# Kernel optimization log

Hardware: AMD Instinct MI355X
Metric: run time of the kernel (lower is better)

## Reference

```python
import jax, jax.numpy as jnp
import numpy as np

UP = 2

def _rect_1d(N, cutoff, edge_val):
    # ideal LPF rect in frequency domain (as in alias_free_convnets ideal_lpf.py)
    lo = int((N * cutoff) // 2)
    hi = int(N - lo)
    r = np.ones(N, dtype=np.float32)
    r[lo + 1:hi] = 0.0
    if (cutoff * N) % 2 == 0:
        r[lo] = edge_val
        r[hi] = edge_val
    return r

def _rect_mask_rfft(N, cutoff, edge_val):
    # 2D separable rect mask, cropped to rfft width N//2+1 (assumes square HxW)
    r = _rect_1d(N, cutoff, edge_val)
    m = r[:, None] * r[None, :]
    return jnp.asarray(m[:, :N // 2 + 1])

def _upsample_rfft(x):
    # x: [B, C, H, W] channels-first. Zero-insertion upsample by UP, then
    # ideal reconstruction LPF in rfft domain (recon rect has edge value 1).
    B, C, H, W = x.shape
    z = jnp.zeros((B, C, H, UP, W, UP), x.dtype)
    z = z.at[:, :, :, 0, :, 0].set(x)
    xu = z.reshape(B, C, H * UP, W * UP)
    mask = _rect_mask_rfft(W * UP, 1.0 / UP, 1.0)
    xf = jnp.fft.rfft2(xu) * (UP * UP) * mask
    return jnp.fft.irfft2(xf, s=(H * UP, W * UP)).astype(x.dtype)

def _lpf_rfft(x, cutoff=0.5):
    # ideal low-pass filter in rfft domain (lpf rect has edge value 0.5)
    H, W = x.shape[-2], x.shape[-1]
    mask = _rect_mask_rfft(W, cutoff, 0.5)
    xf = jnp.fft.rfft2(x) * mask
    return jnp.fft.irfft2(xf, s=(H, W)).astype(x.dtype)

def setup_inputs() -> dict:
    key = jax.random.key(0)
    ks = jax.random.split(key, 6)
    B, H, W, dim = 16, 64, 64, 96
    hidden = 4 * dim  # expand_ratio * dim
    x = jax.random.normal(ks[0], (B, H, W, dim), jnp.float32)
    W1 = jax.random.normal(ks[1], (hidden, dim), jnp.float32) * 0.02
    b1 = jnp.zeros((hidden,), jnp.float32)
    W2 = jax.random.normal(ks[2], (dim, hidden), jnp.float32) * 0.02
    b2 = jnp.zeros((dim,), jnp.float32)
    # PolyActPerChannel default coefficients, repeated per channel: [hidden, 3]
    init_coef = jnp.asarray([0.0169394634313126, 0.5, 0.3078363963999393], jnp.float32)
    coef = jnp.tile(init_coef[None, :], (hidden, 1))
    return {"x": x, "W1": W1, "b1": b1, "W2": W2, "b2": b2, "coef": coef}

def reference(x, W1, b1, W2, b2, coef):
    # x: [B, H, W, C] channels-last
    xc = jnp.transpose(x, (0, 3, 1, 2))            # [B, C, H, W]
    xu = _upsample_rfft(xc)                        # [B, C, 2H, 2W]
    h = jnp.transpose(xu, (0, 2, 3, 1))            # [B, 2H, 2W, C]
    h = h @ W1.T + b1                              # pwconv1 -> [B, 2H, 2W, 4C]
    # per-channel degree-2 polynomial activation
    h = coef[:, 0] + coef[:, 1] * h + coef[:, 2] * (h * h)
    h = h @ W2.T + b2                              # pwconv2 -> [B, 2H, 2W, C]
    hc = jnp.transpose(h, (0, 3, 1, 2))            # [B, C, 2H, 2W]
    hl = _lpf_rfft(hc, cutoff=0.5)                 # anti-alias LPF
    out = hl[:, :, ::2, ::2]                       # stride-2 downsample
    return jnp.transpose(out, (0, 2, 3, 1))        # [B, H, W, C]
```

## Files before the change

kernel.cpp:

```cpp
#include <hip/hip_runtime.h>
#include <hip/hip_bf16.h>

typedef __hip_bfloat16 bf16;
typedef __bf16 bf16x8 __attribute__((ext_vector_type(8)));
typedef float f32x16 __attribute__((ext_vector_type(16)));

union Frag { uint4 q; bf16x8 v; unsigned short us[8]; };

#define PI_D 3.14159265358979323846

__device__ __forceinline__ unsigned short bfbits(float x){ bf16 h = __float2bfloat16(x); return *(unsigned short*)&h; }
__device__ __forceinline__ float frombits(unsigned short b){ union{float f; unsigned u;}v; v.u = ((unsigned)b)<<16; return v.f; }

#define GLD_LDS16(gp, lp) __builtin_amdgcn_global_load_lds( \
    (const __attribute__((address_space(1))) unsigned int*)(gp), \
    (__attribute__((address_space(3))) unsigned int*)(lp), 16, 0, 0)

__global__ void k_init(const float* __restrict__ W1, const float* __restrict__ b1,
                       const float* __restrict__ W2, const float* __restrict__ b2,
                       const float* __restrict__ coef,
                       bf16* __restrict__ W1f, bf16* __restrict__ W2A2f,
                       float* __restrict__ rtab, float* __restrict__ bias2p) {
    int idx = blockIdx.x * 256 + threadIdx.x;
    if (idx < 96) {
        float acc = b2[idx];
        for (int h = 0; h < 384; ++h) {
            float bb = b1[h], C0 = coef[h*3], C1 = coef[h*3+1], C2 = coef[h*3+2];
            float A0 = C0 + C1 * bb + C2 * bb * bb;
            acc += W2[idx * 384 + h] * A0;
        }
        bias2p[idx] = acc;
    }
    if (idx < 384) {
        float bb = b1[idx], C1 = coef[idx*3+1], C2 = coef[idx*3+2];
        rtab[idx] = (C1 + 2.f * C2 * bb) / C2;
    }
    if (idx < 36864) {
        int j = idx & 7, lane = (idx >> 3) & 63, rest = idx >> 9;
        int g2 = lane >> 5;
        {
            int s = rest % 6, ht = rest / 6;
            int p = lane & 31;
            int b = p >> 2, m4 = b & 3; if (m4 == 1 || m4 == 2) b ^= 3;
            int h = ht * 32 + ((b << 2) | (p & 3));
            int k = s * 16 + g2 * 8 + j;
            W1f[idx] = __float2bfloat16(W1[h * 96 + k]);
        }
        {
            int s = rest & 1, rest2 = rest >> 1;
            int ct = rest2 % 3, ht = rest2 / 3;
            int c = ct * 32 + (lane & 31);
            int h = ht * 32 + s * 16 + g2 * 8 + j;
            float C2 = coef[h*3+2];
            W2A2f[idx] = __float2bfloat16(W2[c * 384 + h] * C2);
        }
    }
}

__global__ void k_init2(bf16* __restrict__ upA, bf16* __restrict__ lpA) {
    int idx = blockIdx.x * 256 + threadIdx.x;
    int e = (idx < 12288) ? idx : idx - 12288;
    int j = e & 7, lane = (e >> 3) & 63, mt = (e >> 9) & 1, step = e >> 10;
    int m = 32 * mt + (lane & 31);
    int p = (step & 3) * 16 + (lane >> 5) * 8 + j;
    int d2 = 2 * (m - p);
    int n = ((idx < 12288) ? (d2 + 1) : (d2 - 1)) & 127;
    double s = 1.0;
    for (int k = 1; k <= 31; ++k) s += 2.0 * cos((2.0 * PI_D / 128.0) * (double)k * (double)n);
    float F = (float)(s / ((idx < 12288) ? 64.0 : 128.0));
    bf16 fh = __float2bfloat16(F);
    bf16 val = (step < 8) ? fh : __float2bfloat16(F - __bfloat162float(fh));
    (idx < 12288 ? upA : lpA)[((step * 2 + mt) * 64 + lane) * 8 + j] = val;
}

__device__ __forceinline__ void fir_load_a12(const uint4* __restrict__ atab,
                                             int lane, int mt, Frag af[12]) {
    #pragma unroll
    for (int s = 0; s < 12; ++s) af[s].q = atab[(s * 2 + mt) * 64 + lane];
}
__device__ __forceinline__ void fir_load_a8(const uint4* __restrict__ atab,
                                            int lane, int mt, Frag af[8]) {
    #pragma unroll
    for (int s = 0; s < 8; ++s) {
        int st = (s < 4) ? s : (s + 4);
        af[s].q = atab[(st * 2 + mt) * 64 + lane];
    }
}

__device__ __forceinline__ f32x16 fir_gemm(const Frag af[12],
                                           const unsigned char* BtS,
                                           int lane, int nt) {
    const int n = 32 * nt + (lane & 31);
    const int rowbase = n * 256;
    const int swz = (n & 7) << 4;
    const int g16 = (lane >> 5) * 16;
    f32x16 C;
    #pragma unroll
    for (int e = 0; e < 16; ++e) C[e] = 0.f;
    #pragma unroll
    for (int s = 0; s < 12; ++s) {
        int k2 = (s & 3) * 32 + (((s >> 2) == 1) ? 128 : 0) + g16;
        Frag bf_;
        bf_.q = *(const uint4*)(BtS + rowbase + (k2 ^ swz));
        C = __builtin_amdgcn_mfma_f32_32x32x16_bf16(af[s].v, bf_.v, C, 0, 0, 0);
    }
    return C;
}

__device__ __forceinline__ f32x16 fir_gemm_h(const Frag af[8],
                                             const unsigned char* BtS,
                                             int lane, int nt) {
    const int n = 32 * nt + (lane & 31);
    const int rowbase = n * 128;
    const int swz = (n & 7) << 4;
    const int g16 = (lane >> 5) * 16;
    f32x16 C;
    #pragma unroll
    for (int e = 0; e < 16; ++e) C[e] = 0.f;
    #pragma unroll
    for (int s = 0; s < 8; ++s) {
        int k2 = (s & 3) * 32 + g16;
        Frag bf_;
        bf_.q = *(const uint4*)(BtS + rowbase + (k2 ^ swz));
        C = __builtin_amdgcn_mfma_f32_32x32x16_bf16(af[s].v, bf_.v, C, 0, 0, 0);
    }
    return C;
}

__global__ __launch_bounds__(384, 2) void k_up_v(const float* __restrict__ x,
                                                 const uint4* __restrict__ atab,
                                                 bf16* __restrict__ t1) {
    __shared__ __align__(16) unsigned char BtS[24576];
    __shared__ __align__(16) float xe[64 * 96];
    __shared__ float As[96];
    const int tid = threadIdx.x;
    const int lane = tid & 63, w = tid >> 6;
    const int b = blockIdx.x >> 6, q = blockIdx.x & 63;
    Frag af[12];
    fir_load_a12(atab, lane, w / 3, af);
    for (int g = tid; g < 768; g += 384) {
        int pp = g / 24, c4 = (g - pp * 24) * 4;
        const float* xsrc = &x[((b * 64 + 2 * pp) * 64 + q) * 96 + c4];
        float4 v0 = *(const float4*)xsrc;
        float4 v1 = *(const float4*)(xsrc + 6144);
        *(float4*)&xe[(2 * pp) * 96 + c4] = v0;
        *(float4*)&xe[(2 * pp + 1) * 96 + c4] = v1;
        float f0a[4] = {v0.x, v0.y, v0.z, v0.w};
        float f1a[4] = {v1.x, v1.y, v1.z, v1.w};
        #pragma unroll
        for (int e = 0; e < 4; ++e) {
            int n = c4 + e;
            unsigned short h0 = bfbits(f0a[e]), h1 = bfbits(f1a[e]);
            unsigned short l0 = bfbits(f0a[e] - frombits(h0));
            unsigned short l1 = bfbits(f1a[e] - frombits(h1));
            int base = n * 256 + ((4 * pp) ^ ((n & 7) << 4));
            *(unsigned*)(BtS + base) = (unsigned)h0 | ((unsigned)h1 << 16);
            *(unsigned*)(BtS + base + 128) = (unsigned)l0 | ((unsigned)l1 << 16);
        }
    }
    __syncthreads();
    if (tid < 96) {
        float a = 0.f;
        for (int p = 0; p < 64; p += 2) a += xe[p * 96 + tid] - xe[(p + 1) * 96 + tid];
        As[tid] = a * 0.015625f;
    }
    __syncthreads();
    f32x16 C = fir_gemm(af, BtS, lane, w % 3);
    bf16* dst = t1 + (size_t)b * 786432 + (size_t)q * 96;
    const int c = 32 * (w % 3) + (lane & 31);
    #pragma unroll
    for (int r = 0; r < 16; ++r) {
        int m = 32 * (w / 3) + (r & 3) + 8 * (r >> 2) + 4 * (lane >> 5);
        dst[(size_t)(2 * m + 1) * 6144 + c] = __float2bfloat16(C[r]);
    }
    for (int g = tid; g < 1536; g += 384) {
        int u = g / 24, c4 = (g - u * 24) * 4;
        float sgn = (u & 1) ? -1.f : 1.f;
        float4 xv = *(const float4*)&xe[u * 96 + c4];
        float4 av = *(const float4*)&As[c4];
        uint2 pk;
        pk.x = (unsigned)bfbits(fmaf(sgn, av.x, xv.x)) | ((unsigned)bfbits(fmaf(sgn, av.y, xv.y)) << 16);
        pk.y = (unsigned)bfbits(fmaf(sgn, av.z, xv.z)) | ((unsigned)bfbits(fmaf(sgn, av.w, xv.w)) << 16);
        *(uint2*)&dst[(size_t)(2 * u) * 6144 + c4] = pk;
    }
}

__global__ __launch_bounds__(384, 2) void k_up_h(const bf16* __restrict__ t1,
                                                 const uint4* __restrict__ atab,
                                                 bf16* __restrict__ xu) {
    __shared__ __align__(16) unsigned char BtS[96 * 128];
    __shared__ __align__(16) bf16 xe[64 * 96];
    __shared__ float As[96];
    const int tid = threadIdx.x;
    const int lane = tid & 63, w = tid >> 6;
    const size_t row = blockIdx.x;
    const bf16* src = t1 + row * 6144;
    Frag af[8];
    fir_load_a8(atab, lane, w / 3, af);
    {
        int pp = tid / 12, c8 = (tid - pp * 12) * 8;
        const bf16* s0 = src + (2 * pp) * 96 + c8;
        uint4 v0 = *(const uint4*)s0;
        uint4 v1 = *(const uint4*)(s0 + 96);
        *(uint4*)&xe[(2 * pp) * 96 + c8] = v0;
        *(uint4*)&xe[(2 * pp + 1) * 96 + c8] = v1;
        const unsigned short* u0 = (const unsigned short*)&v0;
        const unsigned short* u1 = (const unsigned short*)&v1;
        #pragma unroll
        for (int e = 0; e < 8; ++e) {
            int n = c8 + e;
            int base = n * 128 + ((4 * pp) ^ ((n & 7) << 4));
            *(unsigned*)(BtS + base) = (unsigned)u0[e] | ((unsigned)u1[e] << 16);
        }
    }
    __syncthreads();
    if (tid < 96) {
        float a = 0.f;
        for (int p = 0; p < 64; p += 2)
            a += __bfloat162float(xe[p * 96 + tid]) - __bfloat162float(xe[(p + 1) * 96 + tid]);
        As[tid] = a * 0.015625f;
    }
    __syncthreads();
    f32x16 C = fir_gemm_h(af, BtS, lane, w % 3);
    bf16* dst = xu + row * 12288;
    const int c = 32 * (w % 3) + (lane & 31);
    #pragma unroll
    for (int r = 0; r < 16; ++r) {
        int m = 32 * (w / 3) + (r & 3) + 8 * (r >> 2) + 4 * (lane >> 5);
        dst[(2 * m + 1) * 96 + c] = __float2bfloat16(C[r]);
    }
    for (int g = tid; g < 1536; g += 384) {
        int v = g / 24, c4 = (g - v * 24) * 4;
        float sgn = (v & 1) ? -1.f : 1.f;
        uint2 xv = *(const uint2*)&xe[v * 96 + c4];
        const unsigned short* us = (const unsigned short*)&xv;
        uint2 pk;
        pk.x = (unsigned)bfbits(fmaf(sgn, As[c4 + 0], frombits(us[0])))
             | ((unsigned)bfbits(fmaf(sgn, As[c4 + 1], frombits(us[1]))) << 16);
        pk.y = (unsigned)bfbits(fmaf(sgn, As[c4 + 2], frombits(us[2])))
             | ((unsigned)bfbits(fmaf(sgn, As[c4 + 3], frombits(us[3]))) << 16);
        *(uint2*)&dst[(2 * v) * 96 + c4] = pk;
    }
}

__global__ __launch_bounds__(512, 2) void k_mlp(const bf16* __restrict__ xu,
                                                const uint4* __restrict__ W1f,
                                                const uint4* __restrict__ W2A2f,
                                                const float* __restrict__ rtabg,
                                                const float* __restrict__ bias2p,
                                                bf16* __restrict__ y) {
    extern __shared__ __align__(16) uint4 wAll[];
    float* rtabL = (float*)(wAll + 144 * 64);
    const int tid = threadIdx.x;
    const int lane = tid & 63;
    const int w = tid >> 6;
    const int half = w & 1;
    const int rw = w >> 1;
    const int lm = lane & 31;
    const int g = lane >> 5;
    const size_t row = (size_t)blockIdx.x * 4 + rw;

    #pragma unroll 2
    for (int c0 = 0; c0 < 144; c0 += 8) {
        int c = c0 + w;
        const uint4* gp = (c < 72) ? (W1f + (size_t)c * 64)
                                   : (W2A2f + (size_t)(c - 72) * 64);
        GLD_LDS16(gp + lane, &wAll[c * 64]);
    }
    if (tid < 96) GLD_LDS16(rtabg + tid * 4, rtabL + tid * 4);

    Frag xr0[6], xr1[6];
    const bf16* xb0 = xu + row * 12288 + (size_t)(half * 64 + lm) * 96 + g * 8;
    const bf16* xb1 = xb0 + 32 * 96;
    #pragma unroll
    for (int s = 0; s < 6; ++s) { xr0[s].q = *(const uint4*)(xb0 + 16 * s);
                                  xr1[s].q = *(const uint4*)(xb1 + 16 * s); }

    asm volatile("s_waitcnt vmcnt(0)" ::: "memory");
    __syncthreads();

    f32x16 ya0[3], ya1[3];
    #pragma unroll
    for (int ct = 0; ct < 3; ++ct) {
        #pragma unroll
        for (int e = 0; e < 16; ++e) { ya0[ct][e] = 0.f; ya1[ct][e] = 0.f; }
    }

    for (int ht = 0; ht < 12; ++ht) {
        const float* rt = rtabL + ht * 32 + g * 8;
        float4 r00 = *(const float4*)(rt);
        float4 r01 = *(const float4*)(rt + 4);
        float4 r10 = *(const float4*)(rt + 16);
        float4 r11 = *(const float4*)(rt + 20);
        float rr[16] = {r00.x, r00.y, r00.z, r00.w, r01.x, r01.y, r01.z, r01.w,
                        r10.x, r10.y, r10.z, r10.w, r11.x, r11.y, r11.z, r11.w};
        f32x16 d0, d1;
        #pragma unroll
        for (int e = 0; e < 16; ++e) { d0[e] = 0.f; d1[e] = 0.f; }
        #pragma unroll
        for (int s = 0; s < 6; ++s) {
            Frag a; a.q = wAll[(ht * 6 + s) * 64 + lane];
            d0 = __builtin_amdgcn_mfma_f32_32x32x16_bf16(a.v, xr0[s].v, d0, 0, 0, 0);
            d1 = __builtin_amdgcn_mfma_f32_32x32x16_bf16(a.v, xr1[s].v, d1, 0, 0, 0);
        }
        Frag be0[2], be1[2];
        #pragma unroll
        for (int s2 = 0; s2 < 2; ++s2) {
            #pragma unroll
            for (int j = 0; j < 8; ++j) {
                float rv = rr[s2 * 8 + j];
                float v0 = d0[s2 * 8 + j], v1 = d1[s2 * 8 + j];
                be0[s2].v[j] = (__bf16)(v0 * (v0 + rv));
                be1[s2].v[j] = (__bf16)(v1 * (v1 + rv));
            }
        }
        #pragma unroll
        for (int u = 0; u < 6; ++u) {
            int ct = u >> 1, s2 = u & 1;
            Frag a2; a2.q = wAll[(72 + ht * 6 + u) * 64 + lane];
            ya0[ct] = __builtin_amdgcn_mfma_f32_32x32x16_bf16(a2.v, (s2 ? be0[1] : be0[0]).v, ya0[ct], 0, 0, 0);
            ya1[ct] = __builtin_amdgcn_mfma_f32_32x32x16_bf16(a2.v, (s2 ? be1[1] : be1[0]).v, ya1[ct], 0, 0, 0);
        }
    }
    bf16* yb0 = y + row * 12288 + (size_t)(half * 64 + lm) * 96;
    bf16* yb1 = yb0 + 32 * 96;
    #pragma unroll
    for (int ct = 0; ct < 3; ++ct) {
        #pragma unroll
        for (int t = 0; t < 8; ++t) {
            int cbase = 32 * ct + 8 * (t >> 1) + 2 * (t & 1) + 4 * g;
            float bb0 = bias2p[cbase], bb1 = bias2p[cbase + 1];
            unsigned pk0 = (unsigned)bfbits(ya0[ct][2*t] + bb0) | ((unsigned)bfbits(ya0[ct][2*t+1] + bb1) << 16);
            unsigned pk1 = (unsigned)bfbits(ya1[ct][2*t] + bb0) | ((unsigned)bfbits(ya1[ct][2*t+1] + bb1) << 16);
            *(unsigned*)(yb0 + cbase) = pk0;
            *(unsigned*)(yb1 + cbase) = pk1;
        }
    }
}

__global__ __launch_bounds__(384, 2) void k_lpf_v(const bf16* __restrict__ y,
                                                  const uint4* __restrict__ atab,
                                                  bf16* __restrict__ t2) {
    __shared__ __align__(16) unsigned char BtS[192 * 128];
    __shared__ __align__(16) bf16 xe[64 * 192];
    const int tid = threadIdx.x;
    const int lane = tid & 63, w = tid >> 6;
    const int b = blockIdx.x >> 6, j2 = blockIdx.x & 63;
    for (int g = tid; g < 1536; g += 384) {
        int ie = g / 24, rem = g - ie * 24, col = rem / 12, c8 = (rem - col * 12) * 8;
        uint4 v = *(const uint4*)(y + ((size_t)((b * 128 + 2 * ie) * 128 + 2 * j2 + col)) * 96 + c8);
        *(uint4*)&xe[ie * 192 + col * 96 + c8] = v;
    }
    for (int g = tid; g < 768; g += 384) {
        int q_ = g / 24, rem = g - q_ * 24, col = rem / 12, c8 = (rem - col * 12) * 8;
        const bf16* yb = y + ((size_t)((b * 128 + 4 * q_ + 1) * 128 + 2 * j2 + col)) * 96 + c8;
        uint4 v0 = *(const uint4*)yb;
        uint4 v1 = *(const uint4*)(yb + 2 * 12288);
        int np = col * 96 + c8;
        const unsigned short* u0 = (const unsigned short*)&v0;
        const unsigned short* u1 = (const unsigned short*)&v1;
        #pragma unroll
        for (int e = 0; e < 8; ++e) {
            int n = np + e;
            int base = n * 128 + ((4 * q_) ^ ((n & 7) << 4));
            *(unsigned*)(BtS + base) = (unsigned)u0[e] | ((unsigned)u1[e] << 16);
        }
    }
    __syncthreads();
    const int n = 32 * w + (lane & 31);
    const int rowbase = n * 128;
    const int swz = (n & 7) << 4;
    const int g16 = (lane >> 5) * 16;
    f32x16 C0, C1;
    #pragma unroll
    for (int e = 0; e < 16; ++e) { C0[e] = 0.f; C1[e] = 0.f; }
    #pragma unroll
    for (int s = 0; s < 4; ++s) {
        Frag bf_; bf_.q = *(const uint4*)(BtS + rowbase + ((s * 32 + g16) ^ swz));
        Frag a0h; a0h.q = atab[(s * 2 + 0) * 64 + lane];
        Frag a1h; a1h.q = atab[(s * 2 + 1) * 64 + lane];
        Frag a0l; a0l.q = atab[((8 + s) * 2 + 0) * 64 + lane];
        Frag a1l; a1l.q = atab[((8 + s) * 2 + 1) * 64 + lane];
        C0 = __builtin_amdgcn_mfma_f32_32x32x16_bf16(a0h.v, bf_.v, C0, 0, 0, 0);
        C1 = __builtin_amdgcn_mfma_f32_32x32x16_bf16(a1h.v, bf_.v, C1, 0, 0, 0);
        C0 = __builtin_amdgcn_mfma_f32_32x32x16_bf16(a0l.v, bf_.v, C0, 0, 0, 0);
        C1 = __builtin_amdgcn_mfma_f32_32x32x16_bf16(a1l.v, bf_.v, C1, 0, 0, 0);
    }
    const int col = n / 96;
    const int c = n - col * 96;
    const int j = 2 * j2 + col;
    #pragma unroll
    for (int r = 0; r < 16; ++r) {
        int mrow = (r & 3) + 8 * (r >> 2) + 4 * (lane >> 5);
        t2[(size_t)((b * 64 + mrow) * 128 + j) * 96 + c] =
            __float2bfloat16(C0[r] + 0.5f * __bfloat162float(xe[mrow * 192 + n]));
        t2[(size_t)((b * 64 + 32 + mrow) * 128 + j) * 96 + c] =
            __float2bfloat16(C1[r] + 0.5f * __bfloat162float(xe[(32 + mrow) * 192 + n]));
    }
}

__global__ __launch_bounds__(384, 2) void k_lpf_h(const bf16* __restrict__ t2,
                                                  const uint4* __restrict__ atab,
                                                  float* __restrict__ out) {
    __shared__ __align__(16) unsigned char BtS[96 * 128];
    __shared__ __align__(16) bf16 xe[64 * 96];
    const int tid = threadIdx.x;
    const int lane = tid & 63, w = tid >> 6;
    const size_t row = blockIdx.x;
    const bf16* src = t2 + row * 12288;
    Frag af[8];
    fir_load_a8(atab, lane, w / 3, af);
    for (int g = tid; g < 768; g += 384) {
        int ce = g / 12, c8 = (g - ce * 12) * 8;
        uint4 v = *(const uint4*)(src + (2 * ce) * 96 + c8);
        *(uint4*)&xe[ce * 96 + c8] = v;
    }
    {
        int q_ = tid / 12, c8 = (tid - q_ * 12) * 8;
        const bf16* s0 = src + (4 * q_ + 1) * 96 + c8;
        uint4 v0 = *(const uint4*)s0;
        uint4 v1 = *(const uint4*)(s0 + 2 * 96);
        const unsigned short* u0 = (const unsigned short*)&v0;
        const unsigned short* u1 = (const unsigned short*)&v1;
        #pragma unroll
        for (int e = 0; e < 8; ++e) {
            int n = c8 + e;
            int base = n * 128 + ((4 * q_) ^ ((n & 7) << 4));
            *(unsigned*)(BtS + base) = (unsigned)u0[e] | ((unsigned)u1[e] << 16);
        }
    }
    __syncthreads();
    f32x16 C = fir_gemm_h(af, BtS, lane, w % 3);
    const int c = 32 * (w % 3) + (lane & 31);
    #pragma unroll
    for (int r = 0; r < 16; ++r) {
        int m = 32 * (w / 3) + (r & 3) + 8 * (r >> 2) + 4 * (lane >> 5);
        out[row * 6144 + (size_t)m * 96 + c] = C[r] + 0.5f * __bfloat162float(xe[m * 96 + c]);
    }
}

extern "C" void kernel_launch(void* const* d_in, const int* in_sizes, int n_in,
                              void* d_out, int out_size, void* d_ws, size_t ws_size,
                              hipStream_t stream) {
    const float* x    = (const float*)d_in[0];
    const float* W1   = (const float*)d_in[1];
    const float* b1   = (const float*)d_in[2];
    const float* W2   = (const float*)d_in[3];
    const float* b2   = (const float*)d_in[4];
    const float* coef = (const float*)d_in[5];
    float* out = (float*)d_out;

    char* w = (char*)d_ws;
    float* bias2p = (float*)(w);
    bf16*  W1f    = (bf16*)(w + 512);
    bf16*  W2A2f  = (bf16*)(w + 74240);
    float* rtab   = (float*)(w + 147968);
    bf16*  atabU  = (bf16*)(w + 149504);
    bf16*  atabL  = (bf16*)(w + 174080);
    bf16* t1 = (bf16*)(w + 270848);
    bf16* yv = (bf16*)(w + 270848);
    bf16* xu = (bf16*)(w + 100934144);
    bf16* t2 = (bf16*)(w + 100934144);

    k_init <<<144, 256, 0, stream>>>(W1, b1, W2, b2, coef, W1f, W2A2f, rtab, bias2p);
    k_init2<<<96, 256, 0, stream>>>(atabU, atabL);
    k_up_v <<<1024, 384, 0, stream>>>(x, (const uint4*)atabU, t1);
    k_up_h <<<2048, 384, 0, stream>>>(t1, (const uint4*)atabU, xu);
    k_mlp  <<<512, 512, 148992, stream>>>(xu, (const uint4*)W1f, (const uint4*)W2A2f,
                                          rtab, bias2p, yv);
    k_lpf_v<<<1024, 384, 0, stream>>>(yv, (const uint4*)atabL, t2);
    k_lpf_h<<<1024, 384, 0, stream>>>(t2, (const uint4*)atabL, out);
}
```

Before: 143.0 us.

## Halve MLP kernel LDS and per-wave tile, read W2 fragments from global

The MLP kernel now stages only W1 fragments and the activation table in shared memory, roughly halving LDS use. W2 fragments are read per iteration from global memory, relying on L2/L1 caching. Each wave now handles one 32-row tile instead of two, each block covers 2 rows instead of 4, and the grid doubles. The goal is higher occupancy (launch bounds raised to 4 blocks) and lower register pressure. The cost is repeated global loads of W2 per wave and less reuse of each weight fragment across MFMAs.

```diff
diff --git a/kernel.cpp b/kernel.cpp
--- a/kernel.cpp
+++ b/kernel.cpp
@@ -243,97 +243,79 @@
     }
 }
 
-__global__ __launch_bounds__(512, 2) void k_mlp(const bf16* __restrict__ xu,
+__global__ __launch_bounds__(512, 4) void k_mlp(const bf16* __restrict__ xu,
                                                 const uint4* __restrict__ W1f,
                                                 const uint4* __restrict__ W2A2f,
                                                 const float* __restrict__ rtabg,
                                                 const float* __restrict__ bias2p,
                                                 bf16* __restrict__ y) {
     extern __shared__ __align__(16) uint4 wAll[];
-    float* rtabL = (float*)(wAll + 144 * 64);
+    float* rtabL = (float*)(wAll + 72 * 64);
     const int tid = threadIdx.x;
     const int lane = tid & 63;
     const int w = tid >> 6;
-    const int half = w & 1;
-    const int rw = w >> 1;
+    const int rw = w >> 2;
+    const int mt = w & 3;
     const int lm = lane & 31;
     const int g = lane >> 5;
-    const size_t row = (size_t)blockIdx.x * 4 + rw;
-
-    #pragma unroll 2
-    for (int c0 = 0; c0 < 144; c0 += 8) {
-        int c = c0 + w;
-        const uint4* gp = (c < 72) ? (W1f + (size_t)c * 64)
-                                   : (W2A2f + (size_t)(c - 72) * 64);
-        GLD_LDS16(gp + lane, &wAll[c * 64]);
-    }
+    const size_t row = (size_t)blockIdx.x * 2 + rw;
+
+    for (int c = w; c < 72; c += 8)
+        GLD_LDS16(W1f + c * 64 + lane, &wAll[c * 64]);
     if (tid < 96) GLD_LDS16(rtabg + tid * 4, rtabL + tid * 4);
 
-    Frag xr0[6], xr1[6];
-    const bf16* xb0 = xu + row * 12288 + (size_t)(half * 64 + lm) * 96 + g * 8;
-    const bf16* xb1 = xb0 + 32 * 96;
-    #pragma unroll
-    for (int s = 0; s < 6; ++s) { xr0[s].q = *(const uint4*)(xb0 + 16 * s);
-                                  xr1[s].q = *(const uint4*)(xb1 + 16 * s); }
+    Frag xr[6];
+    const bf16* xb = xu + row * 12288 + (size_t)(mt * 32 + lm) * 96 + g * 8;
+    #pragma unroll
+    for (int s = 0; s < 6; ++s) xr[s].q = *(const uint4*)(xb + 16 * s);
 
     asm volatile("s_waitcnt vmcnt(0)" ::: "memory");
     __syncthreads();
 
-    f32x16 ya0[3], ya1[3];
+    f32x16 ya[3];
     #pragma unroll
     for (int ct = 0; ct < 3; ++ct) {
         #pragma unroll
-        for (int e = 0; e < 16; ++e) { ya0[ct][e] = 0.f; ya1[ct][e] = 0.f; }
+        for (int e = 0; e < 16; ++e) ya[ct][e] = 0.f;
     }
 
     for (int ht = 0; ht < 12; ++ht) {
-        const float* rt = rtabL + ht * 32 + g * 8;
-        float4 r00 = *(const float4*)(rt);
-        float4 r01 = *(const float4*)(rt + 4);
-        float4 r10 = *(const float4*)(rt + 16);
-        float4 r11 = *(const float4*)(rt + 20);
-        float rr[16] = {r00.x, r00.y, r00.z, r00.w, r01.x, r01.y, r01.z, r01.w,
-                        r10.x, r10.y, r10.z, r10.w, r11.x, r11.y, r11.z, r11.w};
-        f32x16 d0, d1;
-        #pragma unroll
-        for (int e = 0; e < 16; ++e) { d0[e] = 0.f; d1[e] = 0.f; }
+        Frag a2f[6];
+        #pragma unroll
+        for (int u = 0; u < 6; ++u) a2f[u].q = W2A2f[(ht * 6 + u) * 64 + lane];
+        f32x16 d;
+        #pragma unroll
+        for (int e = 0; e < 16; ++e) d[e] = 0.f;
         #pragma unroll
         for (int s = 0; s < 6; ++s) {
             Frag a; a.q = wAll[(ht * 6 + s) * 64 + lane];
-            d0 = __builtin_amdgcn_mfma_f32_32x32x16_bf16(a.v, xr0[s].v, d0, 0, 0, 0);
-            d1 = __builtin_amdgcn_mfma_f32_32x32x16_bf16(a.v, xr1[s].v, d1, 0, 0, 0);
-        }
-        Frag be0[2], be1[2];
+            d = __builtin_amdgcn_mfma_f32_32x32x16_bf16(a.v, xr[s].v, d, 0, 0, 0);
+        }
+        Frag be[2];
         #pragma unroll
         for (int s2 = 0; s2 < 2; ++s2) {
             #pragma unroll
             for (int j = 0; j < 8; ++j) {
-                float rv = rr[s2 * 8 + j];
-                float v0 = d0[s2 * 8 + j], v1 = d1[s2 * 8 + j];
-                be0[s2].v[j] = (__bf16)(v0 * (v0 + rv));
-                be1[s2].v[j] = (__bf16)(v1 * (v1 + rv));
+                float rv = rtabL[ht * 32 + s2 * 16 + g * 8 + j];
+                float v0 = d[s2 * 8 + j];
+                be[s2].v[j] = (__bf16)(v0 * (v0 + rv));
             }
         }
         #pragma unroll
         for (int u = 0; u < 6; ++u) {
-            int ct = u >> 1, s2 = u & 1;
-            Frag a2; a2.q = wAll[(72 + ht * 6 + u) * 64 + lane];
-            ya0[ct] = __builtin_amdgcn_mfma_f32_32x32x16_bf16(a2.v, (s2 ? be0[1] : be0[0]).v, ya0[ct], 0, 0, 0);
-            ya1[ct] = __builtin_amdgcn_mfma_f32_32x32x16_bf16(a2.v, (s2 ? be1[1] : be1[0]).v, ya1[ct], 0, 0, 0);
-        }
-    }
-    bf16* yb0 = y + row * 12288 + (size_t)(half * 64 + lm) * 96;
-    bf16* yb1 = yb0 + 32 * 96;
+            ya[u >> 1] = __builtin_amdgcn_mfma_f32_32x32x16_bf16(
+                a2f[u].v, (u & 1 ? be[1] : be[0]).v, ya[u >> 1], 0, 0, 0);
+        }
+    }
+    bf16* yb = y + row * 12288 + (size_t)(mt * 32 + lm) * 96;
     #pragma unroll
     for (int ct = 0; ct < 3; ++ct) {
         #pragma unroll
         for (int t = 0; t < 8; ++t) {
             int cbase = 32 * ct + 8 * (t >> 1) + 2 * (t & 1) + 4 * g;
             float bb0 = bias2p[cbase], bb1 = bias2p[cbase + 1];
-            unsigned pk0 = (unsigned)bfbits(ya0[ct][2*t] + bb0) | ((unsigned)bfbits(ya0[ct][2*t+1] + bb1) << 16);
-            unsigned pk1 = (unsigned)bfbits(ya1[ct][2*t] + bb0) | ((unsigned)bfbits(ya1[ct][2*t+1] + bb1) << 16);
-            *(unsigned*)(yb0 + cbase) = pk0;
-            *(unsigned*)(yb1 + cbase) = pk1;
+            unsigned pk = (unsigned)bfbits(ya[ct][2*t] + bb0) | ((unsigned)bfbits(ya[ct][2*t+1] + bb1) << 16);
+            *(unsigned*)(yb + cbase) = pk;
         }
     }
 }
@@ -466,7 +448,7 @@
     k_init2<<<96, 256, 0, stream>>>(atabU, atabL);
     k_up_v <<<1024, 384, 0, stream>>>(x, (const uint4*)atabU, t1);
     k_up_h <<<2048, 384, 0, stream>>>(t1, (const uint4*)atabU, xu);
-    k_mlp  <<<512, 512, 148992, stream>>>(xu, (const uint4*)W1f, (const uint4*)W2A2f,
+    k_mlp  <<<1024, 512, 75264, stream>>>(xu, (const uint4*)W1f, (const uint4*)W2A2f,
                                           rtab, bias2p, yv);
     k_lpf_v<<<1024, 384, 0, stream>>>(yv, (const uint4*)atabL, t2);
     k_lpf_h<<<1024, 384, 0, stream>>>(t2, (const uint4*)atabL, out);
```

After: 143.6 us. Within noise of the previous version (+0.4%).
